# Performance work log

Hardware: AMD Instinct MI355X
Metric: run time of the kernel (lower is better)

The kernel has to match this reference:

```python
import jax, jax.numpy as jnp
import numpy as np

B, N, C = 2, 4096, 256
H = 8          # num heads
D = C // H     # head dim = 32
SR = 2         # spatial reduction ratio
HID = 1024     # mixffn hidden = 4*C
EPS = 1e-5


def layernorm(x, g, b):
    mu = jnp.mean(x, axis=-1, keepdims=True)
    var = jnp.mean(jnp.square(x - mu), axis=-1, keepdims=True)
    return (x - mu) * jax.lax.rsqrt(var + EPS) * g + b


def conv2d(x, w, b, stride, pad, groups=1):
    out = jax.lax.conv_general_dilated(
        x, w, (stride, stride), [(pad, pad), (pad, pad)],
        dimension_numbers=("NCHW", "OIHW", "NCHW"), feature_group_count=groups)
    return out + b[None, :, None, None]


def setup_inputs() -> dict:
    key = jax.random.key(0)
    ks = jax.random.split(key, 20)
    s = lambda k, shape, scale=0.02: jax.random.normal(k, shape, jnp.float32) * scale
    return {
        "x": jax.random.normal(ks[0], (B, N, C), jnp.float32),
        "h": 64, "w": 64,
        "ln1_g": jnp.ones((C,), jnp.float32), "ln1_b": jnp.zeros((C,), jnp.float32),
        "q_w": s(ks[1], (C, C)),
        "kv_w": s(ks[2], (2 * C, C)),
        "sr_w": s(ks[3], (C, C, SR, SR)), "sr_b": jnp.zeros((C,), jnp.float32),
        "srn_g": jnp.ones((C,), jnp.float32), "srn_b": jnp.zeros((C,), jnp.float32),
        "proj_w": s(ks[4], (C, C)), "proj_b": jnp.zeros((C,), jnp.float32),
        "ln2_g": jnp.ones((C,), jnp.float32), "ln2_b": jnp.zeros((C,), jnp.float32),
        "fc1_w": s(ks[5], (HID, C)), "fc1_b": jnp.zeros((HID,), jnp.float32),
        "pe_w": s(ks[6], (HID, 1, 3, 3)), "pe_b": jnp.zeros((HID,), jnp.float32),
        "fc2_w": s(ks[7], (C, HID)), "fc2_b": jnp.zeros((C,), jnp.float32),
    }


def reference(x, h, w, ln1_g, ln1_b, q_w, kv_w, sr_w, sr_b, srn_g, srn_b,
              proj_w, proj_b, ln2_g, ln2_b, fc1_w, fc1_b, pe_w, pe_b, fc2_w, fc2_b):
    b_, n_, c_ = x.shape
    # ---- attention branch ----
    xn = layernorm(x, ln1_g, ln1_b)
    q = jnp.einsum("bnc,oc->bno", xn, q_w).reshape(b_, n_, H, D).transpose(0, 2, 1, 3)  # [B,H,N,D]
    # spatial-reduction of KV
    x_kv = xn.reshape(b_, h, w, c_).transpose(0, 3, 1, 2)              # [B,C,h,w]
    x_kv = conv2d(x_kv, sr_w, sr_b, stride=SR, pad=0)                  # [B,C,h/SR,w/SR]
    nkv = (h // SR) * (w // SR)
    x_kv = x_kv.reshape(b_, c_, nkv).transpose(0, 2, 1)                # [B,Nkv,C]
    x_kv = layernorm(x_kv, srn_g, srn_b)
    kv = jnp.einsum("bnc,oc->bno", x_kv, kv_w).reshape(b_, nkv, 2, H, D)
    k = kv[:, :, 0].transpose(0, 2, 1, 3)                              # [B,H,Nkv,D]
    v = kv[:, :, 1].transpose(0, 2, 1, 3)
    scale = D ** -0.5
    att = jax.nn.softmax(jnp.einsum("bhxd,bhyd->bhxy", q, k) * scale, axis=-1)
    o = jnp.einsum("bhxy,bhyd->bhxd", att, v)                          # [B,H,N,D]
    o = o.transpose(0, 2, 1, 3).reshape(b_, n_, c_)
    o = jnp.einsum("bnc,oc->bno", o, proj_w) + proj_b
    x = x + o
    # ---- Mix-FFN branch ----
    xn2 = layernorm(x, ln2_g, ln2_b)
    xf = xn2.reshape(b_, h, w, c_).transpose(0, 3, 1, 2)               # [B,C,h,w]
    xf = jnp.einsum("bchw,oc->bohw", xf, fc1_w) + fc1_b[None, :, None, None]
    xf = conv2d(xf, pe_w, pe_b, stride=1, pad=1, groups=HID)           # depthwise 3x3
    xf = jax.nn.gelu(xf, approximate=False)
    xf = jnp.einsum("bchw,oc->bohw", xf, fc2_w) + fc2_b[None, :, None, None]
    xf = xf.transpose(0, 2, 3, 1).reshape(b_, n_, c_)
    return x + xf
```

## Files before the change

kernel.cpp:

```cpp
#include <hip/hip_runtime.h>
#include <math.h>

constexpr int BB   = 2;
constexpr int NN   = 4096;
constexpr int CCH  = 256;
constexpr int NH   = 8;
constexpr int HD   = 32;
constexpr int GW   = 64;
constexpr int NKV  = 1024;
constexpr int HIDN = 1024;
constexpr float EPSF = 1e-5f;

typedef short  bf16x8 __attribute__((ext_vector_type(8)));
typedef short  bf16x4 __attribute__((ext_vector_type(4)));
typedef float  f32x4  __attribute__((ext_vector_type(4)));

__device__ __forceinline__ short f2bf(float f) {
    unsigned int u = __float_as_uint(f);
    unsigned int r = (u + 0x7FFFu + ((u >> 16) & 1u)) >> 16;
    return (short)r;
}
__device__ __forceinline__ float bf2f(short s) {
    return __uint_as_float(((unsigned int)(unsigned short)s) << 16);
}
__device__ __forceinline__ void gl16(const void* g, void* l) {
    __builtin_amdgcn_global_load_lds(
        (const __attribute__((address_space(1))) void*)g,
        (__attribute__((address_space(3))) void*)l, 16, 0, 0);
}

__global__ __launch_bounds__(256) void prep_kernel(const float* __restrict__ q_w,
                                                   const float* __restrict__ kv_w,
                                                   const float* __restrict__ proj_w,
                                                   const float* __restrict__ fc1_w,
                                                   const float* __restrict__ fc2_w,
                                                   const float* __restrict__ sr_w,
                                                   short* qwb, short* kvwb, short* pjwb,
                                                   short* f1wb, short* f2wb, short* srwb,
                                                   const float* __restrict__ x,
                                                   const float* __restrict__ ln1_g,
                                                   const float* __restrict__ ln1_b,
                                                   short* __restrict__ xn) {
    __shared__ float pa[4], pb[4];
    int t = threadIdx.x;
    if (blockIdx.x < 4096) {
        int i = blockIdx.x * 256 + t;
        if (i < 65536) { qwb[i] = f2bf(q_w[i] * 0.17677669529663687f); return; }
        i -= 65536;
        if (i < 131072) { kvwb[i] = f2bf(kv_w[i]); return; }
        i -= 131072;
        if (i < 65536) { pjwb[i] = f2bf(proj_w[i]); return; }
        i -= 65536;
        if (i < 262144) { f1wb[i] = f2bf(fc1_w[i]); return; }
        i -= 262144;
        if (i < 262144) { f2wb[i] = f2bf(fc2_w[i]); return; }
        i -= 262144;
        {
            int o = i >> 10, rem = i & 1023, c = rem >> 2, q = rem & 3;
            srwb[o * 1024 + q * 256 + c] = f2bf(sr_w[i]);
        }
        return;
    }
    int row = blockIdx.x - 4096;
    float v = x[row * CCH + t];
    float a = v, b = v * v;
#pragma unroll
    for (int off = 32; off > 0; off >>= 1) {
        a += __shfl_xor(a, off);
        b += __shfl_xor(b, off);
    }
    int w = t >> 6;
    if ((t & 63) == 0) { pa[w] = a; pb[w] = b; }
    __syncthreads();
    a = pa[0] + pa[1] + pa[2] + pa[3];
    b = pb[0] + pb[1] + pb[2] + pb[3];
    float mu = a * (1.0f / CCH);
    float var = b * (1.0f / CCH) - mu * mu;
    float rs = rsqrtf(var + EPSF);
    xn[row * CCH + t] = f2bf((v - mu) * rs * ln1_g[t] + ln1_b[t]);
}

template <bool INBF>
__global__ __launch_bounds__(256) void ln_wave(const void* __restrict__ in,
                                               const float* __restrict__ g,
                                               const float* __restrict__ bta,
                                               short* __restrict__ out) {
    int t = threadIdx.x;
    int w = t >> 6, lane = t & 63;
    int row = blockIdx.x * 4 + w;
    float v[4];
    if (INBF) {
        bf16x4 bv = *(const bf16x4*)&((const short*)in)[(size_t)row * CCH + lane * 4];
#pragma unroll
        for (int j = 0; j < 4; j++) v[j] = bf2f(bv[j]);
    } else {
        float4 fv = *(const float4*)&((const float*)in)[(size_t)row * CCH + lane * 4];
        v[0] = fv.x; v[1] = fv.y; v[2] = fv.z; v[3] = fv.w;
    }
    float a = v[0] + v[1] + v[2] + v[3];
    float b = v[0]*v[0] + v[1]*v[1] + v[2]*v[2] + v[3]*v[3];
#pragma unroll
    for (int off = 1; off < 64; off <<= 1) {
        a += __shfl_xor(a, off);
        b += __shfl_xor(b, off);
    }
    float mu = a * (1.0f / CCH);
    float var = b * (1.0f / CCH) - mu * mu;
    float rs = rsqrtf(var + EPSF);
    bf16x4 ov;
#pragma unroll
    for (int j = 0; j < 4; j++)
        ov[j] = f2bf((v[j] - mu) * rs * g[lane * 4 + j] + bta[lane * 4 + j]);
    *(bf16x4*)&out[(size_t)row * CCH + lane * 4] = ov;
}

template <bool OUTB, int RESMODE>
__global__ __launch_bounds__(256, 4) void gemm64(const short* __restrict__ A,
                                                 const short* __restrict__ W,
                                                 const float* __restrict__ bias,
                                                 const void* __restrict__ res,
                                                 void* __restrict__ outp,
                                                 int M, int O, int K) {
    __shared__ short As0[64][64], Ws0[64][64];
    __shared__ short As1[64][64], Ws1[64][64];
    int t = threadIdx.x;
    int m0 = blockIdx.y * 64, o0 = blockIdx.x * 64;
    int w = t >> 6, lane = t & 63;
    int wm = (w >> 1) * 32, wn = (w & 1) * 32;
    int fr = lane & 15, fq = lane >> 4;
    int srow = lane >> 3;
    int sg   = (lane & 7) ^ srow;
    f32x4 acc[2][2];
#pragma unroll
    for (int mi = 0; mi < 2; mi++)
#pragma unroll
        for (int ni = 0; ni < 2; ni++)
            acc[mi][ni] = f32x4{0.f, 0.f, 0.f, 0.f};

    auto stage = [&](short (*Asb)[64], short (*Wsb)[64], int k0) {
#pragma unroll
        for (int r = 0; r < 2; r++) {
            int rowA = r * 32 + w * 8 + srow;
            gl16(&A[(size_t)(m0 + rowA) * K + k0 + sg * 8], &Asb[r * 32 + w * 8][0]);
            gl16(&W[(size_t)(o0 + rowA) * K + k0 + sg * 8], &Wsb[r * 32 + w * 8][0]);
        }
    };
    auto compute = [&](short (*Asb)[64], short (*Wsb)[64]) {
#pragma unroll
        for (int half = 0; half < 2; half++) {
            bf16x8 af[2], wf[2];
#pragma unroll
            for (int mi = 0; mi < 2; mi++) {
                int row = wm + mi * 16 + fr;
                af[mi] = *(const bf16x8*)&Asb[row][(((half << 2) | fq) ^ (row & 7)) * 8];
            }
#pragma unroll
            for (int ni = 0; ni < 2; ni++) {
                int row = wn + ni * 16 + fr;
                wf[ni] = *(const bf16x8*)&Wsb[row][(((half << 2) | fq) ^ (row & 7)) * 8];
            }
#pragma unroll
            for (int mi = 0; mi < 2; mi++)
#pragma unroll
                for (int ni = 0; ni < 2; ni++)
                    acc[mi][ni] = __builtin_amdgcn_mfma_f32_16x16x32_bf16(
                        af[mi], wf[ni], acc[mi][ni], 0, 0, 0);
        }
    };

    stage(As0, Ws0, 0);
    __syncthreads();
    for (int k0 = 0; k0 < K; k0 += 128) {
        if (k0 + 64 < K) stage(As1, Ws1, k0 + 64);
        compute(As0, Ws0);
        __syncthreads();
        if (k0 + 128 < K) stage(As0, Ws0, k0 + 128);
        if (k0 + 64 < K) compute(As1, Ws1);
        __syncthreads();
    }
#pragma unroll
    for (int mi = 0; mi < 2; mi++)
#pragma unroll
        for (int ni = 0; ni < 2; ni++)
#pragma unroll
            for (int r = 0; r < 4; r++) {
                int m = m0 + wm + mi * 16 + fq * 4 + r;
                int o = o0 + wn + ni * 16 + fr;
                float v = acc[mi][ni][r];
                if (bias) v += bias[o];
                if (RESMODE == 1) v += ((const float*)res)[(size_t)m * O + o];
                if (RESMODE == 2) v += bf2f(((const short*)res)[(size_t)m * O + o]);
                if (OUTB) ((short*)outp)[(size_t)m * O + o] = f2bf(v);
                else      ((float*)outp)[(size_t)m * O + o] = v;
            }
}

__global__ __launch_bounds__(256, 4) void sr_gemm(const short* __restrict__ xn,
                                                  const short* __restrict__ Wsr,
                                                  const float* __restrict__ sr_b,
                                                  float* __restrict__ srtmp) {
    __shared__ short As0[32][64], Ws0[64][64];
    __shared__ short As1[32][64], Ws1[64][64];
    int t = threadIdx.x;
    int m0 = blockIdx.y * 32, o0 = blockIdx.x * 64;
    int w = t >> 6, lane = t & 63;
    int wm = (w >> 1) * 16, wn = (w & 1) * 32;
    int fr = lane & 15, fq = lane >> 4;
    int srow = lane >> 3;
    int sg   = (lane & 7) ^ srow;
    int arow = w * 8 + srow;
    int p = m0 + arow;
    int b = p >> 10, pp = p & 1023, ii = pp >> 5, jj = pp & 31;
    int nbase = ii * 128 + jj * 2;
    size_t xbase = (size_t)(b * NN) * CCH;
    f32x4 acc[2];
    acc[0] = f32x4{0.f, 0.f, 0.f, 0.f};
    acc[1] = f32x4{0.f, 0.f, 0.f, 0.f};

    auto stage = [&](short (*Asb)[64], short (*Wsb)[64], int k0) {
        int q = k0 >> 8, c0 = k0 & 255;
        int n = nbase + (q >> 1) * 64 + (q & 1);
        gl16(&xn[xbase + (size_t)n * CCH + c0 + sg * 8], &Asb[w * 8][0]);
#pragma unroll
        for (int r = 0; r < 2; r++)
            gl16(&Wsr[(size_t)(o0 + r * 32 + w * 8 + srow) * 1024 + k0 + sg * 8],
                 &Wsb[r * 32 + w * 8][0]);
    };
    auto compute = [&](short (*Asb)[64], short (*Wsb)[64]) {
#pragma unroll
        for (int half = 0; half < 2; half++) {
            int cg = (half << 2) | fq;
            int rowa = wm + fr;
            bf16x8 af = *(const bf16x8*)&Asb[rowa][(cg ^ (rowa & 7)) * 8];
            bf16x8 wf[2];
#pragma unroll
            for (int ni = 0; ni < 2; ni++) {
                int row = wn + ni * 16 + fr;
                wf[ni] = *(const bf16x8*)&Wsb[row][(cg ^ (row & 7)) * 8];
            }
#pragma unroll
            for (int ni = 0; ni < 2; ni++)
                acc[ni] = __builtin_amdgcn_mfma_f32_16x16x32_bf16(
                    af, wf[ni], acc[ni], 0, 0, 0);
        }
    };

    stage(As0, Ws0, 0);
    __syncthreads();
    for (int k0 = 0; k0 < 1024; k0 += 128) {
        if (k0 + 64 < 1024) stage(As1, Ws1, k0 + 64);
        compute(As0, Ws0);
        __syncthreads();
        if (k0 + 128 < 1024) stage(As0, Ws0, k0 + 128);
        compute(As1, Ws1);
        __syncthreads();
    }
#pragma unroll
    for (int ni = 0; ni < 2; ni++)
#pragma unroll
        for (int r = 0; r < 4; r++) {
            int m = m0 + wm + fq * 4 + r;
            int o = o0 + wn + ni * 16 + fr;
            srtmp[(size_t)m * CCH + o] = acc[ni][r] + sr_b[o];
        }
}

__global__ __launch_bounds__(256, 2) void gemm_fc1(const short* __restrict__ A,
                                                   const short* __restrict__ W,
                                                   const float* __restrict__ bias,
                                                   short* __restrict__ outp,
                                                   int M, int O, int K) {
    __shared__ short As0[128][64], Ws0[128][64];
    __shared__ short As1[128][64], Ws1[128][64];
    int t = threadIdx.x;
    int m0 = blockIdx.y * 128, o0 = blockIdx.x * 128;
    int w = t >> 6, lane = t & 63;
    int wm = (w >> 1) * 64, wn = (w & 1) * 64;
    int fr = lane & 15, fq = lane >> 4;
    int srow = lane >> 3;
    int sg   = (lane & 7) ^ srow;
    f32x4 acc[4][4];
#pragma unroll
    for (int mi = 0; mi < 4; mi++)
#pragma unroll
        for (int ni = 0; ni < 4; ni++)
            acc[mi][ni] = f32x4{0.f, 0.f, 0.f, 0.f};

    auto stage = [&](short (*Asb)[64], short (*Wsb)[64], int k0) {
#pragma unroll
        for (int r = 0; r < 4; r++) {
            int rowA = r * 32 + w * 8 + srow;
            gl16(&A[(size_t)(m0 + rowA) * K + k0 + sg * 8], &Asb[r * 32 + w * 8][0]);
            gl16(&W[(size_t)(o0 + rowA) * K + k0 + sg * 8], &Wsb[r * 32 + w * 8][0]);
        }
    };
    auto compute = [&](short (*Asb)[64], short (*Wsb)[64]) {
#pragma unroll
        for (int half = 0; half < 2; half++) {
            bf16x8 af[4], wf[4];
#pragma unroll
            for (int mi = 0; mi < 4; mi++) {
                int row = wm + mi * 16 + fr;
                af[mi] = *(const bf16x8*)&Asb[row][(((half << 2) | fq) ^ (row & 7)) * 8];
            }
#pragma unroll
            for (int ni = 0; ni < 4; ni++) {
                int row = wn + ni * 16 + fr;
                wf[ni] = *(const bf16x8*)&Wsb[row][(((half << 2) | fq) ^ (row & 7)) * 8];
            }
#pragma unroll
            for (int mi = 0; mi < 4; mi++)
#pragma unroll
                for (int ni = 0; ni < 4; ni++)
                    acc[mi][ni] = __builtin_amdgcn_mfma_f32_16x16x32_bf16(
                        af[mi], wf[ni], acc[mi][ni], 0, 0, 0);
        }
    };

    stage(As0, Ws0, 0);
    __syncthreads();
    for (int k0 = 0; k0 < K; k0 += 128) {
        if (k0 + 64 < K) stage(As1, Ws1, k0 + 64);
        compute(As0, Ws0);
        __syncthreads();
        if (k0 + 128 < K) stage(As0, Ws0, k0 + 128);
        if (k0 + 64 < K) compute(As1, Ws1);
        __syncthreads();
    }
#pragma unroll
    for (int mi = 0; mi < 4; mi++)
#pragma unroll
        for (int ni = 0; ni < 4; ni++)
#pragma unroll
            for (int r = 0; r < 4; r++) {
                int m = m0 + wm + mi * 16 + fq * 4 + r;
                int o = o0 + wn + ni * 16 + fr;
                outp[(size_t)m * O + o] = f2bf(acc[mi][ni][r] + bias[o]);
            }
}

__global__ __launch_bounds__(256, 4) void kv_gemm(const short* __restrict__ A,
                                                  const short* __restrict__ W,
                                                  short* __restrict__ kvk,
                                                  short* __restrict__ vt) {
    __shared__ short As0[64][64], Ws0[64][64];
    __shared__ short As1[64][64], Ws1[64][64];
    int t = threadIdx.x;
    int m0 = blockIdx.y * 64, o0 = blockIdx.x * 64;
    int w = t >> 6, lane = t & 63;
    int wm = (w >> 1) * 32, wn = (w & 1) * 32;
    int fr = lane & 15, fq = lane >> 4;
    int srow = lane >> 3;
    int sg   = (lane & 7) ^ srow;
    f32x4 acc[2][2];
#pragma unroll
    for (int mi = 0; mi < 2; mi++)
#pragma unroll
        for (int ni = 0; ni < 2; ni++)
            acc[mi][ni] = f32x4{0.f, 0.f, 0.f, 0.f};

    auto stage = [&](short (*Asb)[64], short (*Wsb)[64], int k0) {
#pragma unroll
        for (int r = 0; r < 2; r++) {
            int rowA = r * 32 + w * 8 + srow;
            gl16(&A[(size_t)(m0 + rowA) * CCH + k0 + sg * 8], &Asb[r * 32 + w * 8][0]);
            gl16(&W[(size_t)(o0 + rowA) * CCH + k0 + sg * 8], &Wsb[r * 32 + w * 8][0]);
        }
    };
    auto compute = [&](short (*Asb)[64], short (*Wsb)[64]) {
#pragma unroll
        for (int half = 0; half < 2; half++) {
            bf16x8 af[2], wf[2];
#pragma unroll
            for (int mi = 0; mi < 2; mi++) {
                int row = wm + mi * 16 + fr;
                af[mi] = *(const bf16x8*)&Asb[row][(((half << 2) | fq) ^ (row & 7)) * 8];
            }
#pragma unroll
            for (int ni = 0; ni < 2; ni++) {
                int row = wn + ni * 16 + fr;
                wf[ni] = *(const bf16x8*)&Wsb[row][(((half << 2) | fq) ^ (row & 7)) * 8];
            }
#pragma unroll
            for (int mi = 0; mi < 2; mi++)
#pragma unroll
                for (int ni = 0; ni < 2; ni++)
                    acc[mi][ni] = __builtin_amdgcn_mfma_f32_16x16x32_bf16(
                        af[mi], wf[ni], acc[mi][ni], 0, 0, 0);
        }
    };

    stage(As0, Ws0, 0);
    __syncthreads();
    stage(As1, Ws1, 64);
    compute(As0, Ws0);
    __syncthreads();
    stage(As0, Ws0, 128);
    compute(As1, Ws1);
    __syncthreads();
    stage(As1, Ws1, 192);
    compute(As0, Ws0);
    __syncthreads();
    compute(As1, Ws1);

#pragma unroll
    for (int mi = 0; mi < 2; mi++)
#pragma unroll
        for (int ni = 0; ni < 2; ni++) {
            int o = o0 + wn + ni * 16 + fr;
            int mbase = m0 + wm + mi * 16 + fq * 4;
            if (o < 256) {
#pragma unroll
                for (int r = 0; r < 4; r++)
                    kvk[(size_t)(mbase + r) * 256 + o] = f2bf(acc[mi][ni][r]);
            } else {
                int h = (o - 256) >> 5, d = (o - 256) & 31;
                int b = mbase >> 10, y0 = mbase & 1023;
                bf16x4 pv;
#pragma unroll
                for (int r = 0; r < 4; r++) pv[r] = f2bf(acc[mi][ni][r]);
                *(bf16x4*)&vt[((size_t)((b * NH + h) * HD) + d) * NKV + y0] = pv;
            }
        }
}

__global__ __launch_bounds__(256, 4) void attn_mfma(const short* __restrict__ qb,
                                                    const short* __restrict__ kvk,
                                                    const short* __restrict__ vt,
                                                    short* __restrict__ o) {
    int blk = blockIdx.x;
    int qt = blk & 63; int hh = (blk >> 6) & 7; int b = blk >> 9;
    int t = threadIdx.x; int w = t >> 6; int lane = t & 63;
    int fr = lane & 15, fq = lane >> 4;
    __shared__ short Ks0[128][32], Ks1[128][32];
    __shared__ short Vt0[64][64],  Vt1[64][64];
    __shared__ short Ps[4][16][64];
    int n0 = qt * 64 + w * 16;
    bf16x8 qa = *(const bf16x8*)&qb[((size_t)(b * NN) + n0 + fr) * CCH + hh * HD + fq * 8];
    f32x4 oacc[2];
    float lst[4] = {0.f, 0.f, 0.f, 0.f};
#pragma unroll
    for (int nd = 0; nd < 2; nd++) oacc[nd] = f32x4{0.f, 0.f, 0.f, 0.f};

    int srowK = lane >> 2;
    int sgK   = (lane & 3) ^ (srowK & 3);
    int srowV = lane >> 3;
    int sgV   = (lane & 7) ^ srowV;

    auto stageKV = [&](short (*Ksb)[32], short (*Vtb)[64], int y0) {
#pragma unroll
        for (int r2 = 0; r2 < 2; r2++) {
            int rowK = r2 * 64 + w * 16 + srowK;
            gl16(&kvk[((size_t)(b * NKV) + y0 + rowK) * 256 + hh * HD + sgK * 8],
                 &Ksb[r2 * 64 + w * 16][0]);
        }
#pragma unroll
        for (int r3 = 0; r3 < 2; r3++) {
            int d = w * 8 + srowV;
            gl16(&vt[((size_t)((b * NH + hh) * HD) + d) * NKV + y0 + r3 * 64 + sgV * 8],
                 &Vtb[r3 * 32 + w * 8][0]);
        }
    };
    auto tile = [&](short (*Ksb)[32], short (*Vtb)[64]) {
#pragma unroll
        for (int h2 = 0; h2 < 2; h2++) {
            f32x4 s[4];
#pragma unroll
            for (int ni = 0; ni < 4; ni++) {
                int rowk = h2 * 64 + ni * 16 + fr;
                bf16x8 kb = *(const bf16x8*)&Ksb[rowk][(fq ^ (fr & 3)) * 8];
                s[ni] = __builtin_amdgcn_mfma_f32_16x16x32_bf16(
                    qa, kb, f32x4{0.f, 0.f, 0.f, 0.f}, 0, 0, 0);
            }
#pragma unroll
            for (int r = 0; r < 4; r++) {
                int row = fq * 4 + r;
                float psum = 0.f;
#pragma unroll
                for (int i = 0; i < 4; i++) {
                    float p = __expf(fminf(s[i][r], 30.f));
                    psum += p;
                    int col = i * 16 + fr;
                    int sgp = ((col >> 3) ^ row) & 7;
                    Ps[w][row][sgp * 8 + (col & 7)] = f2bf(p);
                }
                lst[r] += psum;
            }
#pragma unroll
            for (int ks = 0; ks < 2; ks++) {
                int gk = ks * 4 + fq;
                bf16x8 pa = *(const bf16x8*)&Ps[w][fr][((gk ^ fr) & 7) * 8];
#pragma unroll
                for (int nd = 0; nd < 2; nd++) {
                    int rowv = nd * 16 + fr;
                    bf16x8 vb = *(const bf16x8*)&Vtb[h2 * 32 + rowv][((gk ^ (rowv & 7)) & 7) * 8];
                    oacc[nd] = __builtin_amdgcn_mfma_f32_16x16x32_bf16(
                        pa, vb, oacc[nd], 0, 0, 0);
                }
            }
        }
    };

    stageKV(Ks0, Vt0, 0);
    __syncthreads();
    for (int y0 = 0; y0 < NKV; y0 += 256) {
        if (y0 + 128 < NKV) stageKV(Ks1, Vt1, y0 + 128);
        tile(Ks0, Vt0);
        __syncthreads();
        if (y0 + 256 < NKV) stageKV(Ks0, Vt0, y0 + 256);
        tile(Ks1, Vt1);
        __syncthreads();
    }
#pragma unroll
    for (int r = 0; r < 4; r++) {
        float ls = lst[r];
#pragma unroll
        for (int off = 1; off < 16; off <<= 1)
            ls += __shfl_xor(ls, off);
        float inv = 1.f / ls;
        int row = n0 + fq * 4 + r;
#pragma unroll
        for (int nd = 0; nd < 2; nd++)
            o[((size_t)(b * NN) + row) * CCH + hh * HD + nd * 16 + fr] =
                f2bf(oacc[nd][r] * inv);
    }
}

__global__ __launch_bounds__(256, 2) void dwconv_gelu(const short* __restrict__ xf,
                                                      const float* __restrict__ pe_w,
                                                      const float* __restrict__ pe_b,
                                                      short* __restrict__ out) {
    int blk = blockIdx.x;
    int cg = blk & 15, sp = (blk >> 4) & 15, b = blk >> 8;
    int r0 = (sp >> 2) * 16, c0 = (sp & 3) * 16;
    int ch0 = cg * 64;
    int t = threadIdx.x;
    __shared__ short tile[18][18][64];
    for (int idx = t; idx < 18 * 18 * 8; idx += 256) {
        int pix = idx >> 3, part = idx & 7;
        int row = pix / 18, col = pix - row * 18;
        int gr = r0 + row - 1, gc = c0 + col - 1;
        bf16x8 v = {0, 0, 0, 0, 0, 0, 0, 0};
        if (gr >= 0 && gr < 64 && gc >= 0 && gc < 64)
            v = *(const bf16x8*)&xf[((size_t)(b * NN) + gr * GW + gc) * HIDN + ch0 + part * 8];
        *(bf16x8*)&tile[row][col][part * 8] = v;
    }
    __syncthreads();
    int cl = t & 63, sg = t >> 6;
    int ch = ch0 + cl;
    float wv[9];
#pragma unroll
    for (int k = 0; k < 9; k++) wv[k] = pe_w[ch * 9 + k];
    float bias = pe_b[ch];
#pragma unroll
    for (int q = 0; q < 4; q++) {
        int lr = sg * 4 + q;
        float cA[3], cB[3], cC[3];
#pragma unroll
        for (int ki = 0; ki < 3; ki++) {
            cA[ki] = bf2f(tile[lr + ki][0][cl]);
            cB[ki] = bf2f(tile[lr + ki][1][cl]);
        }
        for (int cc = 0; cc < 16; cc++) {
#pragma unroll
            for (int ki = 0; ki < 3; ki++) cC[ki] = bf2f(tile[lr + ki][cc + 2][cl]);
            float acc = bias;
#pragma unroll
            for (int ki = 0; ki < 3; ki++)
                acc += cA[ki] * wv[ki * 3] + cB[ki] * wv[ki * 3 + 1] + cC[ki] * wv[ki * 3 + 2];
            float z = 0.7978845608f * (acc + 0.044715f * acc * acc * acc);
            float e = __expf(-2.f * fabsf(z));
            float th = (1.f - e) / (1.f + e);
            th = (z < 0.f) ? -th : th;
            float gg = 0.5f * acc * (1.f + th);
            out[((size_t)(b * NN) + (r0 + lr) * GW + c0 + cc) * HIDN + ch] = f2bf(gg);
#pragma unroll
            for (int ki = 0; ki < 3; ki++) { cA[ki] = cB[ki]; cB[ki] = cC[ki]; }
        }
    }
}

extern "C" void kernel_launch(void* const* d_in, const int* in_sizes, int n_in,
                              void* d_out, int out_size, void* d_ws, size_t ws_size,
                              hipStream_t stream) {
    const float* x      = (const float*)d_in[0];
    const float* ln1_g  = (const float*)d_in[3];
    const float* ln1_b  = (const float*)d_in[4];
    const float* q_w    = (const float*)d_in[5];
    const float* kv_w   = (const float*)d_in[6];
    const float* sr_w   = (const float*)d_in[7];
    const float* sr_b   = (const float*)d_in[8];
    const float* srn_g  = (const float*)d_in[9];
    const float* srn_b  = (const float*)d_in[10];
    const float* proj_w = (const float*)d_in[11];
    const float* proj_b = (const float*)d_in[12];
    const float* ln2_g  = (const float*)d_in[13];
    const float* ln2_b  = (const float*)d_in[14];
    const float* fc1_w  = (const float*)d_in[15];
    const float* fc1_b  = (const float*)d_in[16];
    const float* pe_w   = (const float*)d_in[17];
    const float* pe_b   = (const float*)d_in[18];
    const float* fc2_w  = (const float*)d_in[19];
    const float* fc2_b  = (const float*)d_in[20];
    float* out = (float*)d_out;

    char* base = (char*)d_ws;
    short* xn    = (short*)(base);
    short* qb    = (short*)(base + (4ull  << 20));
    float* srtmp = (float*)(base + (12ull << 20));
    short* xkvn  = (short*)(base + (14ull << 20));
    short* kvk   = (short*)(base + (15ull << 20));
    short* vtb   = (short*)(base + (17ull << 20));
    short* obf   = (short*)(base + (18ull << 20));
    short* x1    = (short*)(base + (22ull << 20));
    short* xf1   = (short*)(base + (30ull << 20));
    short* xf2g  = (short*)(base + (46ull << 20));
    short* qwb   = (short*)(base + (62ull << 20));
    short* kvwb  = qwb  + 65536;
    short* pjwb  = kvwb + 131072;
    short* f1wb  = pjwb + 65536;
    short* f2wb  = f1wb + 262144;
    short* srwb  = f2wb + 262144;

    prep_kernel<<<4096 + BB * NN, 256, 0, stream>>>(q_w, kv_w, proj_w, fc1_w, fc2_w, sr_w,
                                                    qwb, kvwb, pjwb, f1wb, f2wb, srwb,
                                                    x, ln1_g, ln1_b, xn);
    {
        dim3 g(CCH / 64, (BB * NN) / 64);
        gemm64<true, 0><<<g, 256, 0, stream>>>(xn, qwb, nullptr, nullptr, qb, BB * NN, CCH, CCH);
    }
    {
        dim3 g(CCH / 64, (BB * NKV) / 32);
        sr_gemm<<<g, 256, 0, stream>>>(xn, srwb, sr_b, srtmp);
    }
    ln_wave<false><<<BB * NKV / 4, 256, 0, stream>>>(srtmp, srn_g, srn_b, xkvn);
    {
        dim3 g(512 / 64, (BB * NKV) / 64);
        kv_gemm<<<g, 256, 0, stream>>>(xkvn, kvwb, kvk, vtb);
    }
    attn_mfma<<<BB * NH * (NN / 64), 256, 0, stream>>>(qb, kvk, vtb, obf);
    {
        dim3 g(CCH / 64, (BB * NN) / 64);
        gemm64<true, 1><<<g, 256, 0, stream>>>(obf, pjwb, proj_b, x, x1, BB * NN, CCH, CCH);
    }
    ln_wave<true><<<BB * NN / 4, 256, 0, stream>>>(x1, ln2_g, ln2_b, xn);
    {
        dim3 g(HIDN / 128, (BB * NN) / 128);
        gemm_fc1<<<g, 256, 0, stream>>>(xn, f1wb, fc1_b, xf1, BB * NN, HIDN, CCH);
    }
    dwconv_gelu<<<BB * 256, 256, 0, stream>>>(xf1, pe_w, pe_b, xf2g);
    {
        dim3 g(CCH / 64, (BB * NN) / 64);
        gemm64<false, 2><<<g, 256, 0, stream>>>(xf2g, f2wb, fc2_b, x1, out, BB * NN, CCH, HIDN);
    }
}
```

Before: 120.0 us.

## Fuse Q and SR GEMMs into one launch; double query rows per attention block

The Q projection GEMM and the spatial-reduction conv GEMM become one kernel launch that branches on block index over a shared LDS pool. This removes a launch and lets the two independent GEMMs run concurrently. The attention kernel now handles 128 query rows per block (two 16-row tiles per wave), so each staged K/V tile is reused twice, halving the grid and K/V reload traffic. The cost is more registers and LDS per block, with occupancy lowered to 3 blocks per CU.

```diff
diff --git a/kernel.cpp b/kernel.cpp
--- a/kernel.cpp
+++ b/kernel.cpp
@@ -115,16 +115,16 @@
 }
 
 template <bool OUTB, int RESMODE>
-__global__ __launch_bounds__(256, 4) void gemm64(const short* __restrict__ A,
-                                                 const short* __restrict__ W,
-                                                 const float* __restrict__ bias,
-                                                 const void* __restrict__ res,
-                                                 void* __restrict__ outp,
-                                                 int M, int O, int K) {
-    __shared__ short As0[64][64], Ws0[64][64];
-    __shared__ short As1[64][64], Ws1[64][64];
+__device__ __forceinline__ void gemm64_body(const short* __restrict__ A,
+                                            const short* __restrict__ W,
+                                            const float* __restrict__ bias,
+                                            const void* __restrict__ res,
+                                            void* __restrict__ outp,
+                                            int M, int O, int K, int bx, int by,
+                                            short (*As0)[64], short (*Ws0)[64],
+                                            short (*As1)[64], short (*Ws1)[64]) {
     int t = threadIdx.x;
-    int m0 = blockIdx.y * 64, o0 = blockIdx.x * 64;
+    int m0 = by * 64, o0 = bx * 64;
     int w = t >> 6, lane = t & 63;
     int wm = (w >> 1) * 32, wn = (w & 1) * 32;
     int fr = lane & 15, fq = lane >> 4;
@@ -195,14 +195,27 @@
             }
 }
 
-__global__ __launch_bounds__(256, 4) void sr_gemm(const short* __restrict__ xn,
-                                                  const short* __restrict__ Wsr,
-                                                  const float* __restrict__ sr_b,
-                                                  float* __restrict__ srtmp) {
-    __shared__ short As0[32][64], Ws0[64][64];
-    __shared__ short As1[32][64], Ws1[64][64];
+template <bool OUTB, int RESMODE>
+__global__ __launch_bounds__(256, 4) void gemm64(const short* __restrict__ A,
+                                                 const short* __restrict__ W,
+                                                 const float* __restrict__ bias,
+                                                 const void* __restrict__ res,
+                                                 void* __restrict__ outp,
+                                                 int M, int O, int K) {
+    __shared__ short As0[64][64], Ws0[64][64];
+    __shared__ short As1[64][64], Ws1[64][64];
+    gemm64_body<OUTB, RESMODE>(A, W, bias, res, outp, M, O, K,
+                               blockIdx.x, blockIdx.y, As0, Ws0, As1, Ws1);
+}
+
+__device__ __forceinline__ void sr_body(const short* __restrict__ xn,
+                                        const short* __restrict__ Wsr,
+                                        const float* __restrict__ sr_b,
+                                        float* __restrict__ srtmp, int bx, int by,
+                                        short (*As0)[64], short (*As1)[64],
+                                        short (*Ws0)[64], short (*Ws1)[64]) {
     int t = threadIdx.x;
-    int m0 = blockIdx.y * 32, o0 = blockIdx.x * 64;
+    int m0 = by * 32, o0 = bx * 64;
     int w = t >> 6, lane = t & 63;
     int wm = (w >> 1) * 16, wn = (w & 1) * 32;
     int fr = lane & 15, fq = lane >> 4;
@@ -263,6 +276,31 @@
             int o = o0 + wn + ni * 16 + fr;
             srtmp[(size_t)m * CCH + o] = acc[ni][r] + sr_b[o];
         }
+}
+
+__global__ __launch_bounds__(256, 4) void qsr_gemm(const short* __restrict__ xn,
+                                                   const short* __restrict__ qwb,
+                                                   short* __restrict__ qb,
+                                                   const short* __restrict__ srwb,
+                                                   const float* __restrict__ sr_b,
+                                                   float* __restrict__ srtmp) {
+    __shared__ short pool[16384];
+    int i = blockIdx.x;
+    if (i < 512) {
+        gemm64_body<true, 0>(xn, qwb, nullptr, nullptr, qb, BB * NN, CCH, CCH,
+                             i & 3, i >> 2,
+                             (short(*)[64])(pool),
+                             (short(*)[64])(pool + 4096),
+                             (short(*)[64])(pool + 8192),
+                             (short(*)[64])(pool + 12288));
+    } else {
+        i -= 512;
+        sr_body(xn, srwb, sr_b, srtmp, i & 3, i >> 2,
+                (short(*)[64])(pool),
+                (short(*)[64])(pool + 2048),
+                (short(*)[64])(pool + 4096),
+                (short(*)[64])(pool + 8192));
+    }
 }
 
 __global__ __launch_bounds__(256, 2) void gemm_fc1(const short* __restrict__ A,
@@ -424,23 +462,31 @@
         }
 }
 
-__global__ __launch_bounds__(256, 4) void attn_mfma(const short* __restrict__ qb,
+__global__ __launch_bounds__(256, 3) void attn_mfma(const short* __restrict__ qb,
                                                     const short* __restrict__ kvk,
                                                     const short* __restrict__ vt,
                                                     short* __restrict__ o) {
     int blk = blockIdx.x;
-    int qt = blk & 63; int hh = (blk >> 6) & 7; int b = blk >> 9;
+    int qt = blk & 31; int hh = (blk >> 5) & 7; int b = blk >> 8;
     int t = threadIdx.x; int w = t >> 6; int lane = t & 63;
     int fr = lane & 15, fq = lane >> 4;
     __shared__ short Ks0[128][32], Ks1[128][32];
     __shared__ short Vt0[64][64],  Vt1[64][64];
-    __shared__ short Ps[4][16][64];
-    int n0 = qt * 64 + w * 16;
-    bf16x8 qa = *(const bf16x8*)&qb[((size_t)(b * NN) + n0 + fr) * CCH + hh * HD + fq * 8];
-    f32x4 oacc[2];
-    float lst[4] = {0.f, 0.f, 0.f, 0.f};
-#pragma unroll
-    for (int nd = 0; nd < 2; nd++) oacc[nd] = f32x4{0.f, 0.f, 0.f, 0.f};
+    __shared__ short Ps[4][2][16][64];
+    int n0 = qt * 128 + w * 16;
+    bf16x8 qa[2];
+#pragma unroll
+    for (int mi = 0; mi < 2; mi++)
+        qa[mi] = *(const bf16x8*)&qb[((size_t)(b * NN) + n0 + mi * 64 + fr) * CCH + hh * HD + fq * 8];
+    f32x4 oacc[2][2];
+    float lst[2][4];
+#pragma unroll
+    for (int mi = 0; mi < 2; mi++) {
+#pragma unroll
+        for (int nd = 0; nd < 2; nd++) oacc[mi][nd] = f32x4{0.f, 0.f, 0.f, 0.f};
+#pragma unroll
+        for (int r = 0; r < 4; r++) lst[mi][r] = 0.f;
+    }
 
     int srowK = lane >> 2;
     int sgK   = (lane & 3) ^ (srowK & 3);
@@ -464,38 +510,41 @@
     auto tile = [&](short (*Ksb)[32], short (*Vtb)[64]) {
 #pragma unroll
         for (int h2 = 0; h2 < 2; h2++) {
-            f32x4 s[4];
-#pragma unroll
-            for (int ni = 0; ni < 4; ni++) {
-                int rowk = h2 * 64 + ni * 16 + fr;
-                bf16x8 kb = *(const bf16x8*)&Ksb[rowk][(fq ^ (fr & 3)) * 8];
-                s[ni] = __builtin_amdgcn_mfma_f32_16x16x32_bf16(
-                    qa, kb, f32x4{0.f, 0.f, 0.f, 0.f}, 0, 0, 0);
-            }
-#pragma unroll
-            for (int r = 0; r < 4; r++) {
-                int row = fq * 4 + r;
-                float psum = 0.f;
-#pragma unroll
-                for (int i = 0; i < 4; i++) {
-                    float p = __expf(fminf(s[i][r], 30.f));
-                    psum += p;
-                    int col = i * 16 + fr;
-                    int sgp = ((col >> 3) ^ row) & 7;
-                    Ps[w][row][sgp * 8 + (col & 7)] = f2bf(p);
+#pragma unroll
+            for (int mi = 0; mi < 2; mi++) {
+                f32x4 s[4];
+#pragma unroll
+                for (int ni = 0; ni < 4; ni++) {
+                    int rowk = h2 * 64 + ni * 16 + fr;
+                    bf16x8 kb = *(const bf16x8*)&Ksb[rowk][(fq ^ (fr & 3)) * 8];
+                    s[ni] = __builtin_amdgcn_mfma_f32_16x16x32_bf16(
+                        qa[mi], kb, f32x4{0.f, 0.f, 0.f, 0.f}, 0, 0, 0);
                 }
-                lst[r] += psum;
-            }
-#pragma unroll
-            for (int ks = 0; ks < 2; ks++) {
-                int gk = ks * 4 + fq;
-                bf16x8 pa = *(const bf16x8*)&Ps[w][fr][((gk ^ fr) & 7) * 8];
-#pragma unroll
-                for (int nd = 0; nd < 2; nd++) {
-                    int rowv = nd * 16 + fr;
-                    bf16x8 vb = *(const bf16x8*)&Vtb[h2 * 32 + rowv][((gk ^ (rowv & 7)) & 7) * 8];
-                    oacc[nd] = __builtin_amdgcn_mfma_f32_16x16x32_bf16(
-                        pa, vb, oacc[nd], 0, 0, 0);
+#pragma unroll
+                for (int r = 0; r < 4; r++) {
+                    int row = fq * 4 + r;
+                    float psum = 0.f;
+#pragma unroll
+                    for (int i = 0; i < 4; i++) {
+                        float p = __expf(fminf(s[i][r], 30.f));
+                        psum += p;
+                        int col = i * 16 + fr;
+                        int sgp = ((col >> 3) ^ row) & 7;
+                        Ps[w][mi][row][sgp * 8 + (col & 7)] = f2bf(p);
+                    }
+                    lst[mi][r] += psum;
+                }
+#pragma unroll
+                for (int ks = 0; ks < 2; ks++) {
+                    int gk = ks * 4 + fq;
+                    bf16x8 pa = *(const bf16x8*)&Ps[w][mi][fr][((gk ^ fr) & 7) * 8];
+#pragma unroll
+                    for (int nd = 0; nd < 2; nd++) {
+                        int rowv = nd * 16 + fr;
+                        bf16x8 vb = *(const bf16x8*)&Vtb[h2 * 32 + rowv][((gk ^ (rowv & 7)) & 7) * 8];
+                        oacc[mi][nd] = __builtin_amdgcn_mfma_f32_16x16x32_bf16(
+                            pa, vb, oacc[mi][nd], 0, 0, 0);
+                    }
                 }
             }
         }
@@ -512,18 +561,20 @@
         __syncthreads();
     }
 #pragma unroll
-    for (int r = 0; r < 4; r++) {
-        float ls = lst[r];
-#pragma unroll
-        for (int off = 1; off < 16; off <<= 1)
-            ls += __shfl_xor(ls, off);
-        float inv = 1.f / ls;
-        int row = n0 + fq * 4 + r;
-#pragma unroll
-        for (int nd = 0; nd < 2; nd++)
-            o[((size_t)(b * NN) + row) * CCH + hh * HD + nd * 16 + fr] =
-                f2bf(oacc[nd][r] * inv);
-    }
+    for (int mi = 0; mi < 2; mi++)
+#pragma unroll
+        for (int r = 0; r < 4; r++) {
+            float ls = lst[mi][r];
+#pragma unroll
+            for (int off = 1; off < 16; off <<= 1)
+                ls += __shfl_xor(ls, off);
+            float inv = 1.f / ls;
+            int row = n0 + mi * 64 + fq * 4 + r;
+#pragma unroll
+            for (int nd = 0; nd < 2; nd++)
+                o[((size_t)(b * NN) + row) * CCH + hh * HD + nd * 16 + fr] =
+                    f2bf(oacc[mi][nd][r] * inv);
+        }
 }
 
 __global__ __launch_bounds__(256, 2) void dwconv_gelu(const short* __restrict__ xf,
@@ -625,20 +676,13 @@
     prep_kernel<<<4096 + BB * NN, 256, 0, stream>>>(q_w, kv_w, proj_w, fc1_w, fc2_w, sr_w,
                                                     qwb, kvwb, pjwb, f1wb, f2wb, srwb,
                                                     x, ln1_g, ln1_b, xn);
-    {
-        dim3 g(CCH / 64, (BB * NN) / 64);
-        gemm64<true, 0><<<g, 256, 0, stream>>>(xn, qwb, nullptr, nullptr, qb, BB * NN, CCH, CCH);
-    }
-    {
-        dim3 g(CCH / 64, (BB * NKV) / 32);
-        sr_gemm<<<g, 256, 0, stream>>>(xn, srwb, sr_b, srtmp);
-    }
+    qsr_gemm<<<768, 256, 0, stream>>>(xn, qwb, qb, srwb, sr_b, srtmp);
     ln_wave<false><<<BB * NKV / 4, 256, 0, stream>>>(srtmp, srn_g, srn_b, xkvn);
     {
         dim3 g(512 / 64, (BB * NKV) / 64);
         kv_gemm<<<g, 256, 0, stream>>>(xkvn, kvwb, kvk, vtb);
     }
-    attn_mfma<<<BB * NH * (NN / 64), 256, 0, stream>>>(qb, kvk, vtb, obf);
+    attn_mfma<<<BB * NH * (NN / 128), 256, 0, stream>>>(qb, kvk, vtb, obf);
     {
         dim3 g(CCH / 64, (BB * NN) / 64);
         gemm64<true, 1><<<g, 256, 0, stream>>>(obf, pjwb, proj_b, x, x1, BB * NN, CCH, CCH);
```

Result: faster. 116.7 us (-2.7%).
